# Kernel tuning notes

Hardware: AMD Instinct MI355X
Metric: run time of the kernel (lower is better)

Reference implementation:

```python
import jax, jax.numpy as jnp
import numpy as np

GROUP_SIZE = 128


def setup_inputs() -> dict:
    key = jax.random.key(0)
    kx, kw = jax.random.split(key)
    x = jax.random.normal(kx, (4, 2048, 4096), dtype=jnp.float32)
    weight = jax.random.normal(kw, (11008, 4096), dtype=jnp.float32) * 0.02
    return {"x": x, "weight": weight}


def reference(x, weight):
    # Training-path forward of OneBitLinear (bias=False, group_size=128):
    # per-128-group L-inf scale, STE-sign binarization, rescale, then dense linear.
    O, I = weight.shape                      # [out, in]
    G = GROUP_SIZE
    wg = weight.reshape(O, I // G, G)        # [out, num_groups, group]
    scales = jnp.clip(jnp.max(jnp.abs(wg), axis=-1, keepdims=True), 1e-8)
    w_sign = jnp.sign(wg / scales)           # {-1, 0, +1}
    w_eff = (w_sign * scales).reshape(O, I)  # effective 1-bit weight in fp32
    # F.linear: x @ w_eff.T  -> [batch, seq, out]
    return jnp.einsum('bsi,oi->bso', x, w_eff)
```

## Files before the change

### kernel.cpp

```cpp
#include <hip/hip_runtime.h>

#define M_DIM 8192
#define K_DIM 4096
#define N_DIM 11008
#define BM 256
#define BN 256
#define BK 64
#define TILES_M (M_DIM / BM)
#define TILES_N (N_DIM / BN)
#define NT (K_DIM / BK)
#define NWG (TILES_M * TILES_N)

typedef __attribute__((ext_vector_type(8))) short bf16x8;
typedef __attribute__((ext_vector_type(4))) float f32x4;
typedef __attribute__((ext_vector_type(8))) unsigned short u16x8;

__device__ __forceinline__ unsigned short f2bf_rne(float f) {
    unsigned int u = __float_as_uint(f);
    unsigned int r = (u + 0x7FFFu + ((u >> 16) & 1u)) >> 16;
    return (unsigned short)r;
}

__device__ __forceinline__ void gload_lds16(const void* g, void* l) {
    __builtin_amdgcn_global_load_lds(
        (const __attribute__((address_space(1))) void*)g,
        (__attribute__((address_space(3))) void*)l, 16, 0, 0);
}

__global__ __launch_bounds__(256) void cast_x_kernel(const float* __restrict__ x,
                                                     unsigned short* __restrict__ xb) {
    size_t t = (size_t)blockIdx.x * 256 + threadIdx.x;
    const float4* p = reinterpret_cast<const float4*>(x) + 2 * t;
    float4 a = p[0];
    float4 b = p[1];
    u16x8 o;
    o[0] = f2bf_rne(a.x); o[1] = f2bf_rne(a.y); o[2] = f2bf_rne(a.z); o[3] = f2bf_rne(a.w);
    o[4] = f2bf_rne(b.x); o[5] = f2bf_rne(b.y); o[6] = f2bf_rne(b.z); o[7] = f2bf_rne(b.w);
    *reinterpret_cast<u16x8*>(xb + 8 * t) = o;
}

__global__ __launch_bounds__(256) void binarize_w_kernel(const float* __restrict__ w,
                                                         unsigned short* __restrict__ weff) {
    size_t t = (size_t)blockIdx.x * 256 + threadIdx.x;
    size_t group = t >> 5;
    int l32 = (int)(t & 31);
    const float4* src = reinterpret_cast<const float4*>(w + group * 128) + l32;
    float4 v = *src;
    float amax = fmaxf(fmaxf(fabsf(v.x), fabsf(v.y)), fmaxf(fabsf(v.z), fabsf(v.w)));
#pragma unroll
    for (int off = 16; off >= 1; off >>= 1)
        amax = fmaxf(amax, __shfl_xor(amax, off));
    float scale = fmaxf(amax, 1e-8f);
    unsigned short pb = f2bf_rne(scale);
    unsigned short nb = (unsigned short)(pb | 0x8000u);
    ushort4 o;
    o.x = (v.x == 0.0f) ? (unsigned short)0 : ((v.x > 0.0f) ? pb : nb);
    o.y = (v.y == 0.0f) ? (unsigned short)0 : ((v.y > 0.0f) ? pb : nb);
    o.z = (v.z == 0.0f) ? (unsigned short)0 : ((v.z > 0.0f) ? pb : nb);
    o.w = (v.w == 0.0f) ? (unsigned short)0 : ((v.w > 0.0f) ? pb : nb);
    *reinterpret_cast<ushort4*>(weff + group * 128 + (size_t)l32 * 4) = o;
}

__global__ __launch_bounds__(512, 2) void gemm_bin_kernel(
        const unsigned short* __restrict__ A,
        const unsigned short* __restrict__ B,
        float* __restrict__ C) {
    __shared__ unsigned short lds[2][2][2][8192];

    const int bid = blockIdx.x;
    const int swz = (bid & 7) * (NWG / 8) + (bid >> 3);
    const int tm = swz / TILES_N;
    const int tn = swz % TILES_N;

    const int tid = threadIdx.x;
    const int wave = tid >> 6;
    const int lane = tid & 63;
    const int wm = wave >> 2;
    const int wn = wave & 3;
    const int l15 = lane & 15;
    const int l4  = lane >> 4;
    const int brow0 = (wn & 1) * 64;

    const int srow  = tid >> 3;
    const int gslot = (tid & 7) ^ (srow & 7);
    const unsigned short* Asrc = A + (size_t)(tm * BM + srow) * K_DIM + gslot * 8;
    const unsigned short* Bsrc = B + (size_t)(tn * BN + srow) * K_DIM + gslot * 8;

    auto stageA = [&](int buf, int half, int kt) {
        const unsigned short* s = Asrc + (size_t)(half * 128) * K_DIM + kt;
        unsigned short* d = &lds[buf][0][half][tid * 8];
        gload_lds16(s, d);
        gload_lds16(s + (size_t)64 * K_DIM, d + 4096);
    };
    auto stageB = [&](int buf, int half, int kt) {
        const unsigned short* s = Bsrc + (size_t)(half * 128) * K_DIM + kt;
        unsigned short* d = &lds[buf][1][half][tid * 8];
        gload_lds16(s, d);
        gload_lds16(s + (size_t)64 * K_DIM, d + 4096);
    };
    auto readfrag = [&](const unsigned short* base, int rowl, int ks) -> bf16x8 {
        return *reinterpret_cast<const bf16x8*>(
            &base[rowl * 64 + (((ks * 4 + l4) ^ (rowl & 7)) * 8)]);
    };

    f32x4 acc[8][4] = {};
    bf16x8 bfA[4][2], bfB[4][2], af0[2][2], af1[2][2];

#define READ_A(DST, BASE, Q)                                                    \
    {                                                                           \
        _Pragma("unroll") for (int r_ = 0; r_ < 2; ++r_) {                      \
            _Pragma("unroll") for (int ks_ = 0; ks_ < 2; ++ks_) {               \
                DST[r_][ks_] = readfrag(BASE, (2 * (Q) + r_) * 16 + l15, ks_);  \
            }                                                                   \
        }                                                                       \
    }
#define READ_B(DST, BASE)                                                       \
    {                                                                           \
        _Pragma("unroll") for (int j_ = 0; j_ < 4; ++j_) {                      \
            _Pragma("unroll") for (int ks_ = 0; ks_ < 2; ++ks_) {               \
                DST[j_][ks_] = readfrag(BASE, brow0 + j_ * 16 + l15, ks_);      \
            }                                                                   \
        }                                                                       \
    }
#define MFMA8(AF, BF, Q, KS)                                                    \
    {                                                                           \
        _Pragma("unroll") for (int r_ = 0; r_ < 2; ++r_) {                      \
            _Pragma("unroll") for (int j_ = 0; j_ < 4; ++j_) {                  \
                acc[2 * (Q) + r_][j_] = __builtin_amdgcn_mfma_f32_16x16x32_bf16(\
                    AF[r_][KS], BF[j_][KS], acc[2 * (Q) + r_][j_], 0, 0, 0);    \
            }                                                                   \
        }                                                                       \
    }

    stageA(0, 0, 0); stageA(0, 1, 0);
    stageB(0, 0, 0); stageB(0, 1, 0);
    stageB(1, 0, BK); stageB(1, 1, BK);
    asm volatile("s_waitcnt vmcnt(4)" ::: "memory");
    __builtin_amdgcn_s_barrier();
    READ_B(bfA, (&lds[0][1][wn >> 1][0]));
    READ_A(af0, (&lds[0][0][wm][0]), 0);

#define KTILE(T, CUR, NXT, BF, BFN)                                             \
    {                                                                           \
        const unsigned short* Ah  = &lds[CUR][0][wm][0];                        \
        const unsigned short* Ahn = &lds[NXT][0][wm][0];                        \
        const unsigned short* Bhn = &lds[NXT][1][wn >> 1][0];                   \
                                                                        \
        if ((T) + 1 < NT) stageA(NXT, 0, ((T) + 1) * BK);                       \
        __builtin_amdgcn_s_setprio(1);                                          \
        MFMA8(af0, BF, 0, 0);                                                   \
        READ_A(af1, Ah, 1);                                                     \
        MFMA8(af0, BF, 0, 1);                                                   \
        __builtin_amdgcn_s_setprio(0);                                          \
        __builtin_amdgcn_s_barrier();                                           \
                                                                        \
        if ((T) + 1 < NT) stageA(NXT, 1, ((T) + 1) * BK);                       \
        __builtin_amdgcn_s_setprio(1);                                          \
        MFMA8(af1, BF, 1, 0);                                                   \
        READ_A(af0, Ah, 2);                                                     \
        MFMA8(af1, BF, 1, 1);                                                   \
        __builtin_amdgcn_s_setprio(0);                                          \
        __builtin_amdgcn_s_barrier();                                           \
                                                                        \
        if ((T) + 2 < NT) stageB(CUR, 0, ((T) + 2) * BK);                       \
        __builtin_amdgcn_s_setprio(1);                                          \
        MFMA8(af0, BF, 2, 0);                                                   \
        READ_A(af1, Ah, 3);                                                     \
        MFMA8(af0, BF, 2, 1);                                                   \
        __builtin_amdgcn_s_setprio(0);                                          \
        if ((T) + 2 < NT) { asm volatile("s_waitcnt vmcnt(2)" ::: "memory"); }  \
        else              { asm volatile("s_waitcnt vmcnt(0)" ::: "memory"); }  \
        __builtin_amdgcn_s_barrier();                                           \
                        \
        if ((T) + 2 < NT) stageB(CUR, 1, ((T) + 2) * BK);                       \
        __builtin_amdgcn_s_setprio(1);                                          \
        MFMA8(af1, BF, 3, 0);                                                   \
        if ((T) + 1 < NT) { READ_B(BFN, Bhn); READ_A(af0, Ahn, 0); }            \
        MFMA8(af1, BF, 3, 1);                                                   \
        __builtin_amdgcn_s_setprio(0);                                          \
        __builtin_amdgcn_s_barrier();                                           \
    }

#pragma unroll 1
    for (int tt = 0; tt < NT; tt += 2) {
        KTILE(tt,     0, 1, bfA, bfB);
        KTILE(tt + 1, 1, 0, bfB, bfA);
    }

    const size_t crow0 = (size_t)tm * BM + wm * 128 + l4 * 4;
    const int ccol0 = tn * BN + wn * 64 + l15;
#pragma unroll
    for (int i = 0; i < 8; ++i) {
#pragma unroll
        for (int j = 0; j < 4; ++j) {
            float* cp = C + (crow0 + i * 16) * N_DIM + ccol0 + j * 16;
#pragma unroll
            for (int r = 0; r < 4; ++r)
                __builtin_nontemporal_store(acc[i][j][r], cp + (size_t)r * N_DIM);
        }
    }
}

extern "C" void kernel_launch(void* const* d_in, const int* in_sizes, int n_in,
                              void* d_out, int out_size, void* d_ws, size_t ws_size,
                              hipStream_t stream) {
    const float* x = (const float*)d_in[0];
    const float* w = (const float*)d_in[1];
    float* out = (float*)d_out;

    unsigned short* xb = (unsigned short*)d_ws;
    unsigned short* weff = (unsigned short*)((char*)d_ws + (size_t)M_DIM * K_DIM * 2);

    cast_x_kernel<<<(M_DIM * K_DIM / 8) / 256, 256, 0, stream>>>(x, xb);
    binarize_w_kernel<<<(N_DIM * K_DIM / 4) / 256, 256, 0, stream>>>(w, weff);
    gemm_bin_kernel<<<NWG, 512, 0, stream>>>(xb, weff, out);
}
```

Baseline: 742.9 us.

## Restructure GEMM main loop into barrier-separated phases with single fragment buffers

Replaces the interleaved LDS-read/MFMA schedule that double-buffered A and B register fragments with eight explicit phases per two k-tiles. Each phase reads its A (and sometimes B) fragments, issues a global-to-LDS stage, waits on lgkmcnt and a barrier, then runs all MFMAs for that quarter. This cuts fragment register usage and simplifies waitcnt handling. In exchange, LDS reads no longer overlap MFMA execution within a wave, and there are more barriers per tile.

```diff
diff --git a/kernel.cpp b/kernel.cpp
--- a/kernel.cpp
+++ b/kernel.cpp
@@ -104,32 +104,50 @@
     };
 
     f32x4 acc[8][4] = {};
-    bf16x8 bfA[4][2], bfB[4][2], af0[2][2], af1[2][2];
-
-#define READ_A(DST, BASE, Q)                                                    \
+    bf16x8 bf[4][2], af[2][2];
+
+#define READ_A(BASE, Q)                                                         \
     {                                                                           \
         _Pragma("unroll") for (int r_ = 0; r_ < 2; ++r_) {                      \
             _Pragma("unroll") for (int ks_ = 0; ks_ < 2; ++ks_) {               \
-                DST[r_][ks_] = readfrag(BASE, (2 * (Q) + r_) * 16 + l15, ks_);  \
+                af[r_][ks_] = readfrag(BASE, (2 * (Q) + r_) * 16 + l15, ks_);   \
             }                                                                   \
         }                                                                       \
     }
-#define READ_B(DST, BASE)                                                       \
+#define READ_B(BASE)                                                            \
     {                                                                           \
         _Pragma("unroll") for (int j_ = 0; j_ < 4; ++j_) {                      \
             _Pragma("unroll") for (int ks_ = 0; ks_ < 2; ++ks_) {               \
-                DST[j_][ks_] = readfrag(BASE, brow0 + j_ * 16 + l15, ks_);      \
+                bf[j_][ks_] = readfrag(BASE, brow0 + j_ * 16 + l15, ks_);       \
             }                                                                   \
         }                                                                       \
     }
-#define MFMA8(AF, BF, Q, KS)                                                    \
-    {                                                                           \
-        _Pragma("unroll") for (int r_ = 0; r_ < 2; ++r_) {                      \
-            _Pragma("unroll") for (int j_ = 0; j_ < 4; ++j_) {                  \
-                acc[2 * (Q) + r_][j_] = __builtin_amdgcn_mfma_f32_16x16x32_bf16(\
-                    AF[r_][KS], BF[j_][KS], acc[2 * (Q) + r_][j_], 0, 0, 0);    \
+#define MFMA_PH(Q)                                                              \
+    {                                                                           \
+        _Pragma("unroll") for (int ks_ = 0; ks_ < 2; ++ks_) {                   \
+            _Pragma("unroll") for (int r_ = 0; r_ < 2; ++r_) {                  \
+                _Pragma("unroll") for (int j_ = 0; j_ < 4; ++j_) {              \
+                    acc[2 * (Q) + r_][j_] =                                     \
+                        __builtin_amdgcn_mfma_f32_16x16x32_bf16(                \
+                            af[r_][ks_], bf[j_][ks_], acc[2 * (Q) + r_][j_],    \
+                            0, 0, 0);                                           \
+                }                                                               \
             }                                                                   \
         }                                                                       \
+    }
+#define PHASE(ABASE, Q, RDB, BBASE, STAGE_STMT, VMSTMT)                         \
+    {                                                                           \
+        READ_A(ABASE, Q);                                                       \
+        if (RDB) { READ_B(BBASE); }                                             \
+        STAGE_STMT;                                                             \
+        if (RDB) { asm volatile("s_waitcnt lgkmcnt(8)" ::: "memory"); }         \
+        __builtin_amdgcn_s_barrier();                                           \
+        asm volatile("s_waitcnt lgkmcnt(0)" ::: "memory");                      \
+        __builtin_amdgcn_s_setprio(1);                                          \
+        MFMA_PH(Q);                                                             \
+        __builtin_amdgcn_s_setprio(0);                                          \
+        VMSTMT;                                                                 \
+        __builtin_amdgcn_s_barrier();                                           \
     }
 
     stageA(0, 0, 0); stageA(0, 1, 0);
@@ -137,54 +155,31 @@
     stageB(1, 0, BK); stageB(1, 1, BK);
     asm volatile("s_waitcnt vmcnt(4)" ::: "memory");
     __builtin_amdgcn_s_barrier();
-    READ_B(bfA, (&lds[0][1][wn >> 1][0]));
-    READ_A(af0, (&lds[0][0][wm][0]), 0);
-
-#define KTILE(T, CUR, NXT, BF, BFN)                                             \
-    {                                                                           \
-        const unsigned short* Ah  = &lds[CUR][0][wm][0];                        \
-        const unsigned short* Ahn = &lds[NXT][0][wm][0];                        \
-        const unsigned short* Bhn = &lds[NXT][1][wn >> 1][0];                   \
-                                                                        \
-        if ((T) + 1 < NT) stageA(NXT, 0, ((T) + 1) * BK);                       \
-        __builtin_amdgcn_s_setprio(1);                                          \
-        MFMA8(af0, BF, 0, 0);                                                   \
-        READ_A(af1, Ah, 1);                                                     \
-        MFMA8(af0, BF, 0, 1);                                                   \
-        __builtin_amdgcn_s_setprio(0);                                          \
-        __builtin_amdgcn_s_barrier();                                           \
-                                                                        \
-        if ((T) + 1 < NT) stageA(NXT, 1, ((T) + 1) * BK);                       \
-        __builtin_amdgcn_s_setprio(1);                                          \
-        MFMA8(af1, BF, 1, 0);                                                   \
-        READ_A(af0, Ah, 2);                                                     \
-        MFMA8(af1, BF, 1, 1);                                                   \
-        __builtin_amdgcn_s_setprio(0);                                          \
-        __builtin_amdgcn_s_barrier();                                           \
-                                                                        \
-        if ((T) + 2 < NT) stageB(CUR, 0, ((T) + 2) * BK);                       \
-        __builtin_amdgcn_s_setprio(1);                                          \
-        MFMA8(af0, BF, 2, 0);                                                   \
-        READ_A(af1, Ah, 3);                                                     \
-        MFMA8(af0, BF, 2, 1);                                                   \
-        __builtin_amdgcn_s_setprio(0);                                          \
-        if ((T) + 2 < NT) { asm volatile("s_waitcnt vmcnt(2)" ::: "memory"); }  \
-        else              { asm volatile("s_waitcnt vmcnt(0)" ::: "memory"); }  \
-        __builtin_amdgcn_s_barrier();                                           \
-                        \
-        if ((T) + 2 < NT) stageB(CUR, 1, ((T) + 2) * BK);                       \
-        __builtin_amdgcn_s_setprio(1);                                          \
-        MFMA8(af1, BF, 3, 0);                                                   \
-        if ((T) + 1 < NT) { READ_B(BFN, Bhn); READ_A(af0, Ahn, 0); }            \
-        MFMA8(af1, BF, 3, 1);                                                   \
-        __builtin_amdgcn_s_setprio(0);                                          \
-        __builtin_amdgcn_s_barrier();                                           \
-    }
 
 #pragma unroll 1
     for (int tt = 0; tt < NT; tt += 2) {
-        KTILE(tt,     0, 1, bfA, bfB);
-        KTILE(tt + 1, 1, 0, bfB, bfA);
+        const unsigned short* A0 = &lds[0][0][wm][0];
+        const unsigned short* B0 = &lds[0][1][wn >> 1][0];
+        const unsigned short* A1 = &lds[1][0][wm][0];
+        const unsigned short* B1 = &lds[1][1][wn >> 1][0];
+        const bool more = (tt + 2 < NT);
+        const int kA1 = (tt + 1) * BK;
+        const int kN2 = (tt + 2) * BK;
+        const int kN3 = (tt + 3) * BK;
+
+        PHASE(A0, 0, 1, B0, { stageA(1, 0, kA1); }, {});
+        PHASE(A0, 1, 0, B0, { stageA(1, 1, kA1); }, {});
+        PHASE(A0, 2, 0, B0, { if (more) stageB(0, 0, kN2); }, {});
+        PHASE(A0, 3, 0, B0, { if (more) stageB(0, 1, kN2); },
+              { if (more) { asm volatile("s_waitcnt vmcnt(4)" ::: "memory"); }
+                else      { asm volatile("s_waitcnt vmcnt(0)" ::: "memory"); } });
+
+        PHASE(A1, 0, 1, B1, { if (more) stageA(0, 0, kN2); }, {});
+        PHASE(A1, 1, 0, B1, { if (more) stageA(0, 1, kN2); }, {});
+        PHASE(A1, 2, 0, B1, { if (more) stageB(1, 0, kN3); }, {});
+        PHASE(A1, 3, 0, B1, { if (more) stageB(1, 1, kN3); },
+              { if (more) { asm volatile("s_waitcnt vmcnt(4)" ::: "memory"); }
+                else      { asm volatile("s_waitcnt vmcnt(0)" ::: "memory"); } });
     }
 
     const size_t crow0 = (size_t)tm * BM + wm * 128 + l4 * 4;
```

After: 744.1 us. About the same (+0.2%).
